# Performance work log

Measured on AMD Instinct MI355X. Metric: run time of the kernel, lower is better.

Reference implementation:

```python
import jax, jax.numpy as jnp
import numpy as np

B, C, H, W = 4, 64, 64, 64
INTER = max(1, C // 8)


def setup_inputs() -> dict:
    key = jax.random.key(0)
    ks = jax.random.split(key, 8)
    return {
        "x": jax.random.normal(ks[0], (B, C, H, W), dtype=jnp.float32),
        "Wq": jax.random.normal(ks[1], (INTER, C), dtype=jnp.float32) * 0.1,
        "bq": jax.random.normal(ks[2], (INTER,), dtype=jnp.float32) * 0.1,
        "Wk": jax.random.normal(ks[3], (INTER, C), dtype=jnp.float32) * 0.1,
        "bk": jax.random.normal(ks[4], (INTER,), dtype=jnp.float32) * 0.1,
        "Wv": jax.random.normal(ks[5], (C, C), dtype=jnp.float32) * 0.1,
        "bv": jax.random.normal(ks[6], (C,), dtype=jnp.float32) * 0.1,
        "gamma": jax.random.normal(ks[7], (1,), dtype=jnp.float32),
    }


def reference(x, Wq, bq, Wk, bk, Wv, bv, gamma):
    b, c, h, w = x.shape
    n = h * w
    xf = x.reshape(b, c, n)  # flatten spatial dims, [B, C, N]
    # 1x1 convs == per-pixel matmuls
    q = jnp.einsum('ic,bcn->bin', Wq, xf) + bq[None, :, None]  # [B, inter, N]
    k = jnp.einsum('ic,bcn->bin', Wk, xf) + bk[None, :, None]  # [B, inter, N]
    v = jnp.einsum('oc,bcn->bon', Wv, xf) + bv[None, :, None]  # [B, C, N]
    # energy[b,n,m] = sum_i q[b,i,n] * k[b,i,m]  (unscaled attention)
    energy = jnp.einsum('bin,bim->bnm', q, k)  # [B, N, N]
    attn = jax.nn.softmax(energy, axis=-1)
    # out[b,c,n] = sum_m v[b,c,m] * attn[b,n,m]
    out = jnp.einsum('bcm,bnm->bcn', v, attn).reshape(b, c, h, w)
    return gamma[0] * out + x
```

## Files before the change

kernel.cpp:

```cpp
#include <hip/hip_runtime.h>


#define NPIX 4096
typedef __attribute__((ext_vector_type(8))) short s8v;
typedef __attribute__((ext_vector_type(4))) float f4v;

static __device__ __forceinline__ unsigned short f2bf(float f) {
    union { float f; unsigned u; } v; v.f = f;
    unsigned r = v.u + 0x7FFFu + ((v.u >> 16) & 1u);
    return (unsigned short)(r >> 16);
}

extern "C" __global__ void __launch_bounds__(256, 4) qkv_kernel(
    const float* __restrict__ x,
    const float* __restrict__ Wq, const float* __restrict__ bq,
    const float* __restrict__ Wk, const float* __restrict__ bk,
    const float* __restrict__ Wv, const float* __restrict__ bv,
    unsigned short* __restrict__ qt, unsigned short* __restrict__ kt,
    unsigned short* __restrict__ vb)
{
    __shared__ float xs[64][17];
    __shared__ __align__(16) float wls[80][68];
    __shared__ float bls[80];
    const int t = threadIdx.x;
    const int b = blockIdx.x >> 8, n0 = (blockIdx.x & 255) << 4;

    for (int e = t; e < 1024; e += 256) {
        int c = e >> 4, j = e & 15;
        xs[c][j] = x[((b << 6) + c) * NPIX + n0 + j];
    }
    for (int e = t; e < 5120; e += 256) {
        int row = e >> 6, cc = e & 63;
        wls[row][cc] = (e < 512) ? Wq[e] : (e < 1024) ? Wk[e - 512] : Wv[e - 1024];
    }
    if (t < 80) bls[t] = (t < 8) ? bq[t] : (t < 16) ? bk[t - 8] : bv[t - 16];
    __syncthreads();

    const int j = t & 15, oh = t >> 4;
    float xr[64];
#pragma unroll
    for (int c = 0; c < 64; ++c) xr[c] = xs[c][j];

    const int n = n0 + j;
#pragma unroll
    for (int r = 0; r < 5; ++r) {
        const int row = oh * 5 + r;
        float acc = bls[row];
#pragma unroll
        for (int q = 0; q < 16; ++q) {
            float4 wv = *(const float4*)&wls[row][q * 4];
            acc += wv.x * xr[4*q] + wv.y * xr[4*q+1] + wv.z * xr[4*q+2] + wv.w * xr[4*q+3];
        }
        const unsigned short h = f2bf(acc);
        if (row < 8)       qt[(b * NPIX + n) * 8 + row] = h;
        else if (row < 16) kt[(b * NPIX + n) * 8 + row - 8] = h;
        else               vb[((b << 6) + (row - 16)) * NPIX + n] = h;
    }
}

extern "C" __global__ void __launch_bounds__(512, 4) attn_kernel(
    const unsigned short* __restrict__ qt, const unsigned short* __restrict__ kt,
    const unsigned short* __restrict__ vb,
    const float* __restrict__ x, const float* __restrict__ gamma_p,
    float* __restrict__ out)
{
    __shared__ __align__(16) unsigned short vls[4][64][64];
    __shared__ __align__(16) unsigned short pls[8][16][72];
    __shared__ float ored[2][128][17];
    __shared__ float Lred[4][2][16];

    const int t = threadIdx.x;
    const int w = t >> 6, lane = t & 63, g = lane >> 4, c16 = lane & 15;
    const int gg = w >> 1, wg = w & 1;
    const int bid = ((blockIdx.x & 7) << 6) + (blockIdx.x >> 3);
    const int b = bid >> 7, n0 = (bid & 127) << 5;

    const unsigned short* qtB = qt + b * NPIX * 8;
    const unsigned short* ktB = kt + b * NPIX * 8;
    const unsigned short* vbB = vb + (b << 6) * NPIX;

    s8v qfr = {0,0,0,0,0,0,0,0};
    if (g == 0) qfr = *(const s8v*)(qtB + (n0 + wg * 16 + c16) * 8);

    const int t2 = t & 127;
    const int vc = t2 >> 1, hh = t2 & 1;
    const int mbase = gg << 10;

    f4v accO[4];
#pragma unroll
    for (int cs = 0; cs < 4; ++cs) { accO[cs][0]=0.f; accO[cs][1]=0.f; accO[cs][2]=0.f; accO[cs][3]=0.f; }
    float lsum[4] = {0.f, 0.f, 0.f, 0.f};

    s8v vr[4], kf[4], kfn[4];
    {
        const unsigned short* vp = vbB + vc * NPIX + mbase + hh * 32;
        vr[0] = *(const s8v*)(vp);     vr[1] = *(const s8v*)(vp + 8);
        vr[2] = *(const s8v*)(vp + 16); vr[3] = *(const s8v*)(vp + 24);
#pragma unroll
        for (int ms = 0; ms < 4; ++ms) {
            s8v z = {0,0,0,0,0,0,0,0};
            kf[ms] = z;
            if (g == 0) kf[ms] = *(const s8v*)(ktB + (mbase + ms * 16 + c16) * 8);
        }
    }

    for (int ti = 0; ti < 16; ++ti) {
#pragma unroll
        for (int q = 0; q < 4; ++q) {
            const int pos = (hh * 4 + q) ^ (vc & 7);
            *(s8v*)&vls[gg][vc][pos * 8] = vr[q];
        }
        __syncthreads();

        if (ti < 15) {
            const int m1 = mbase + ((ti + 1) << 6);
            const unsigned short* vp = vbB + vc * NPIX + m1 + hh * 32;
            vr[0] = *(const s8v*)(vp);      vr[1] = *(const s8v*)(vp + 8);
            vr[2] = *(const s8v*)(vp + 16); vr[3] = *(const s8v*)(vp + 24);
#pragma unroll
            for (int ms = 0; ms < 4; ++ms) {
                s8v z = {0,0,0,0,0,0,0,0};
                kfn[ms] = z;
                if (g == 0) kfn[ms] = *(const s8v*)(ktB + (m1 + ms * 16 + c16) * 8);
            }
        }

        f4v sm[4];
#pragma unroll
        for (int ms = 0; ms < 4; ++ms) {
            f4v z; z[0]=0.f; z[1]=0.f; z[2]=0.f; z[3]=0.f;
            sm[ms] = __builtin_amdgcn_mfma_f32_16x16x32_bf16(qfr, kf[ms], z, 0, 0, 0);
        }

#pragma unroll
        for (int ms = 0; ms < 4; ++ms)
#pragma unroll
            for (int r = 0; r < 4; ++r) {
                float p = __expf(sm[ms][r]);
                lsum[r] += p;
                pls[w][g * 4 + r][ms * 16 + c16] = f2bf(p);
            }
        __builtin_amdgcn_wave_barrier();

        s8v pf0 = *(const s8v*)&pls[w][c16][g * 8];
        s8v pf1 = *(const s8v*)&pls[w][c16][32 + g * 8];

#pragma unroll
        for (int cs = 0; cs < 4; ++cs) {
            const int c = cs * 16 + c16;
            const int q0 = (g)     ^ (c16 & 7);
            const int q1 = (4 + g) ^ (c16 & 7);
            s8v vf0 = *(const s8v*)&vls[gg][c][q0 * 8];
            s8v vf1 = *(const s8v*)&vls[gg][c][q1 * 8];
            accO[cs] = __builtin_amdgcn_mfma_f32_16x16x32_bf16(vf0, pf0, accO[cs], 0, 0, 0);
            accO[cs] = __builtin_amdgcn_mfma_f32_16x16x32_bf16(vf1, pf1, accO[cs], 0, 0, 0);
        }
        __syncthreads();

#pragma unroll
        for (int ms = 0; ms < 4; ++ms) kf[ms] = kfn[ms];
    }

#pragma unroll
    for (int r = 0; r < 4; ++r) {
        float L = lsum[r];
        L += __shfl_xor(L, 1); L += __shfl_xor(L, 2);
        L += __shfl_xor(L, 4); L += __shfl_xor(L, 8);
        lsum[r] = L;
    }
    if (c16 == 0) {
#pragma unroll
        for (int r = 0; r < 4; ++r) Lred[gg][wg][g * 4 + r] = lsum[r];
    }

    const int s2 = t & 127;
    if (gg >= 2) {
#pragma unroll
        for (int cs = 0; cs < 4; ++cs)
#pragma unroll
            for (int r = 0; r < 4; ++r) ored[gg - 2][s2][cs * 4 + r] = accO[cs][r];
    }
    __syncthreads();
    if (gg < 2) {
#pragma unroll
        for (int cs = 0; cs < 4; ++cs)
#pragma unroll
            for (int r = 0; r < 4; ++r) accO[cs][r] += ored[gg][s2][cs * 4 + r];
    }
    __syncthreads();
    if (gg == 1) {
#pragma unroll
        for (int cs = 0; cs < 4; ++cs)
#pragma unroll
            for (int r = 0; r < 4; ++r) ored[0][s2][cs * 4 + r] = accO[cs][r];
    }
    __syncthreads();
    if (gg == 0) {
#pragma unroll
        for (int cs = 0; cs < 4; ++cs)
#pragma unroll
            for (int r = 0; r < 4; ++r) accO[cs][r] += ored[0][s2][cs * 4 + r];

        const float L = Lred[0][wg][c16] + Lred[1][wg][c16]
                      + Lred[2][wg][c16] + Lred[3][wg][c16];
        const float inv = 1.0f / L;
        const float gm = gamma_p[0];
        const int n = n0 + wg * 16 + c16;
#pragma unroll
        for (int cs = 0; cs < 4; ++cs)
#pragma unroll
            for (int r = 0; r < 4; ++r) {
                const int c = cs * 16 + g * 4 + r;
                const int gi = ((b << 6) + c) * NPIX + n;
                out[gi] = gm * (accO[cs][r] * inv) + x[gi];
            }
    }
}

extern "C" void kernel_launch(void* const* d_in, const int* in_sizes, int n_in,
                              void* d_out, int out_size, void* d_ws, size_t ws_size,
                              hipStream_t stream) {
    const float* x     = (const float*)d_in[0];
    const float* Wq    = (const float*)d_in[1];
    const float* bq    = (const float*)d_in[2];
    const float* Wk    = (const float*)d_in[3];
    const float* bk    = (const float*)d_in[4];
    const float* Wv    = (const float*)d_in[5];
    const float* bv    = (const float*)d_in[6];
    const float* gamma = (const float*)d_in[7];

    unsigned short* qt = (unsigned short*)d_ws;
    unsigned short* kt = qt + 4 * NPIX * 8;
    unsigned short* vb = kt + 4 * NPIX * 8;

    qkv_kernel<<<1024, 256, 0, stream>>>(x, Wq, bq, Wk, bk, Wv, bv, qt, kt, vb);
    attn_kernel<<<512, 512, 0, stream>>>(qt, kt, vb, x, gamma, (float*)d_out);
}
```

Baseline: 112.0 us.

## Restructure attention kernel: direct V fragment loads, 16-query tiles, exp2 softmax

Each attention block now handles 16 query pixels with 4 waves splitting the key range, up from 32 pixels with 8 waves. V fragments are loaded straight from global memory into registers and prefetched one tile ahead, which removes the LDS staging and both per-iteration __syncthreads. Q is pre-scaled by log2(e) in the projection kernel so the softmax can use a hardware exp2. The S MFMA operands are swapped so P can be written to LDS with packed bf16x2 stores, and the end-of-kernel reduction is a single LDS pass with vectorized float4 output. In exchange, V traffic from global/L2 is higher because there are twice as many blocks and no reuse of V through LDS.

```diff
diff --git a/kernel.cpp b/kernel.cpp
--- a/kernel.cpp
+++ b/kernel.cpp
@@ -1,7 +1,9 @@
 #include <hip/hip_runtime.h>
+#include <hip/hip_bf16.h>
 
 
 #define NPIX 4096
+#define LOG2E 1.44269504088896f
 typedef __attribute__((ext_vector_type(8))) short s8v;
 typedef __attribute__((ext_vector_type(4))) float f4v;
 
@@ -9,6 +11,17 @@
     union { float f; unsigned u; } v; v.f = f;
     unsigned r = v.u + 0x7FFFu + ((v.u >> 16) & 1u);
     return (unsigned short)(r >> 16);
+}
+static __device__ __forceinline__ unsigned pkbf2(float a, float b) {
+    __hip_bfloat162 h = __float22bfloat162_rn(make_float2(a, b));
+    return *reinterpret_cast<unsigned*>(&h);
+}
+static __device__ __forceinline__ float fexp2(float x) {
+#if __has_builtin(__builtin_amdgcn_exp2f)
+    return __builtin_amdgcn_exp2f(x);
+#else
+    return exp2f(x);
+#endif
 }
 
 extern "C" __global__ void __launch_bounds__(256, 4) qkv_kernel(
@@ -31,9 +44,10 @@
     }
     for (int e = t; e < 5120; e += 256) {
         int row = e >> 6, cc = e & 63;
-        wls[row][cc] = (e < 512) ? Wq[e] : (e < 1024) ? Wk[e - 512] : Wv[e - 1024];
-    }
-    if (t < 80) bls[t] = (t < 8) ? bq[t] : (t < 16) ? bk[t - 8] : bv[t - 16];
+        float wv = (e < 512) ? Wq[e] * LOG2E : (e < 1024) ? Wk[e - 512] : Wv[e - 1024];
+        wls[row][cc] = wv;
+    }
+    if (t < 80) bls[t] = (t < 8) ? bq[t] * LOG2E : (t < 16) ? bk[t - 8] : bv[t - 16];
     __syncthreads();
 
     const int j = t & 15, oh = t >> 4;
@@ -58,88 +72,76 @@
     }
 }
 
-extern "C" __global__ void __launch_bounds__(512, 4) attn_kernel(
+extern "C" __global__ void __launch_bounds__(256, 4) attn_kernel(
     const unsigned short* __restrict__ qt, const unsigned short* __restrict__ kt,
     const unsigned short* __restrict__ vb,
     const float* __restrict__ x, const float* __restrict__ gamma_p,
     float* __restrict__ out)
 {
-    __shared__ __align__(16) unsigned short vls[4][64][64];
-    __shared__ __align__(16) unsigned short pls[8][16][72];
-    __shared__ float ored[2][128][17];
-    __shared__ float Lred[4][2][16];
+    __shared__ __align__(16) unsigned short pls[4][16][72];
+    __shared__ __align__(16) float Ored[4][64][20];
+    __shared__ __align__(16) float Lr[4][16];
 
     const int t = threadIdx.x;
     const int w = t >> 6, lane = t & 63, g = lane >> 4, c16 = lane & 15;
-    const int gg = w >> 1, wg = w & 1;
-    const int bid = ((blockIdx.x & 7) << 6) + (blockIdx.x >> 3);
-    const int b = bid >> 7, n0 = (bid & 127) << 5;
+    const int raw = blockIdx.x;
+    const int sw = ((raw & 7) << 7) + (raw >> 3);
+    const int b = sw >> 8, n0 = (sw & 255) << 4;
 
     const unsigned short* qtB = qt + b * NPIX * 8;
     const unsigned short* ktB = kt + b * NPIX * 8;
     const unsigned short* vbB = vb + (b << 6) * NPIX;
 
     s8v qfr = {0,0,0,0,0,0,0,0};
-    if (g == 0) qfr = *(const s8v*)(qtB + (n0 + wg * 16 + c16) * 8);
-
-    const int t2 = t & 127;
-    const int vc = t2 >> 1, hh = t2 & 1;
-    const int mbase = gg << 10;
+    if (g == 0) qfr = *(const s8v*)(qtB + (n0 + c16) * 8);
+
+    const int mbase = w << 10;
+    const unsigned short* vrow = vbB + c16 * NPIX + g * 8;
 
     f4v accO[4];
 #pragma unroll
     for (int cs = 0; cs < 4; ++cs) { accO[cs][0]=0.f; accO[cs][1]=0.f; accO[cs][2]=0.f; accO[cs][3]=0.f; }
-    float lsum[4] = {0.f, 0.f, 0.f, 0.f};
-
-    s8v vr[4], kf[4], kfn[4];
-    {
-        const unsigned short* vp = vbB + vc * NPIX + mbase + hh * 32;
-        vr[0] = *(const s8v*)(vp);     vr[1] = *(const s8v*)(vp + 8);
-        vr[2] = *(const s8v*)(vp + 16); vr[3] = *(const s8v*)(vp + 24);
-#pragma unroll
-        for (int ms = 0; ms < 4; ++ms) {
-            s8v z = {0,0,0,0,0,0,0,0};
-            kf[ms] = z;
-            if (g == 0) kf[ms] = *(const s8v*)(ktB + (mbase + ms * 16 + c16) * 8);
-        }
+    float lsum = 0.f;
+
+    s8v kf[4], vf[8];
+#pragma unroll
+    for (int ms = 0; ms < 4; ++ms) {
+        s8v z = {0,0,0,0,0,0,0,0};
+        kf[ms] = z;
+        if (g == 0) kf[ms] = *(const s8v*)(ktB + (mbase + ms * 16 + c16) * 8);
+    }
+#pragma unroll
+    for (int cs = 0; cs < 4; ++cs) {
+        vf[cs*2+0] = *(const s8v*)(vrow + cs * 16 * NPIX + mbase);
+        vf[cs*2+1] = *(const s8v*)(vrow + cs * 16 * NPIX + mbase + 32);
     }
 
     for (int ti = 0; ti < 16; ++ti) {
-#pragma unroll
-        for (int q = 0; q < 4; ++q) {
-            const int pos = (hh * 4 + q) ^ (vc & 7);
-            *(s8v*)&vls[gg][vc][pos * 8] = vr[q];
-        }
-        __syncthreads();
-
-        if (ti < 15) {
-            const int m1 = mbase + ((ti + 1) << 6);
-            const unsigned short* vp = vbB + vc * NPIX + m1 + hh * 32;
-            vr[0] = *(const s8v*)(vp);      vr[1] = *(const s8v*)(vp + 8);
-            vr[2] = *(const s8v*)(vp + 16); vr[3] = *(const s8v*)(vp + 24);
-#pragma unroll
-            for (int ms = 0; ms < 4; ++ms) {
-                s8v z = {0,0,0,0,0,0,0,0};
-                kfn[ms] = z;
-                if (g == 0) kfn[ms] = *(const s8v*)(ktB + (m1 + ms * 16 + c16) * 8);
-            }
-        }
+        const int mg = mbase + (ti << 6);
 
         f4v sm[4];
 #pragma unroll
         for (int ms = 0; ms < 4; ++ms) {
             f4v z; z[0]=0.f; z[1]=0.f; z[2]=0.f; z[3]=0.f;
-            sm[ms] = __builtin_amdgcn_mfma_f32_16x16x32_bf16(qfr, kf[ms], z, 0, 0, 0);
-        }
-
-#pragma unroll
-        for (int ms = 0; ms < 4; ++ms)
-#pragma unroll
-            for (int r = 0; r < 4; ++r) {
-                float p = __expf(sm[ms][r]);
-                lsum[r] += p;
-                pls[w][g * 4 + r][ms * 16 + c16] = f2bf(p);
+            sm[ms] = __builtin_amdgcn_mfma_f32_16x16x32_bf16(kf[ms], qfr, z, 0, 0, 0);
+        }
+
+        if (ti < 15) {
+            const int m1 = mg + 64;
+#pragma unroll
+            for (int ms = 0; ms < 4; ++ms) {
+                if (g == 0) kf[ms] = *(const s8v*)(ktB + (m1 + ms * 16 + c16) * 8);
             }
+        }
+
+#pragma unroll
+        for (int ms = 0; ms < 4; ++ms) {
+            float p0 = fexp2(sm[ms][0]), p1 = fexp2(sm[ms][1]);
+            float p2 = fexp2(sm[ms][2]), p3 = fexp2(sm[ms][3]);
+            lsum += (p0 + p1) + (p2 + p3);
+            uint2 pk; pk.x = pkbf2(p0, p1); pk.y = pkbf2(p2, p3);
+            *(uint2*)&pls[w][c16][ms * 16 + g * 4] = pk;
+        }
         __builtin_amdgcn_wave_barrier();
 
         s8v pf0 = *(const s8v*)&pls[w][c16][g * 8];
@@ -147,73 +149,55 @@
 
 #pragma unroll
         for (int cs = 0; cs < 4; ++cs) {
-            const int c = cs * 16 + c16;
-            const int q0 = (g)     ^ (c16 & 7);
-            const int q1 = (4 + g) ^ (c16 & 7);
-            s8v vf0 = *(const s8v*)&vls[gg][c][q0 * 8];
-            s8v vf1 = *(const s8v*)&vls[gg][c][q1 * 8];
-            accO[cs] = __builtin_amdgcn_mfma_f32_16x16x32_bf16(vf0, pf0, accO[cs], 0, 0, 0);
-            accO[cs] = __builtin_amdgcn_mfma_f32_16x16x32_bf16(vf1, pf1, accO[cs], 0, 0, 0);
-        }
-        __syncthreads();
-
-#pragma unroll
-        for (int ms = 0; ms < 4; ++ms) kf[ms] = kfn[ms];
-    }
-
-#pragma unroll
-    for (int r = 0; r < 4; ++r) {
-        float L = lsum[r];
-        L += __shfl_xor(L, 1); L += __shfl_xor(L, 2);
-        L += __shfl_xor(L, 4); L += __shfl_xor(L, 8);
-        lsum[r] = L;
-    }
-    if (c16 == 0) {
-#pragma unroll
-        for (int r = 0; r < 4; ++r) Lred[gg][wg][g * 4 + r] = lsum[r];
-    }
-
-    const int s2 = t & 127;
-    if (gg >= 2) {
-#pragma unroll
-        for (int cs = 0; cs < 4; ++cs)
-#pragma unroll
-            for (int r = 0; r < 4; ++r) ored[gg - 2][s2][cs * 4 + r] = accO[cs][r];
-    }
+            accO[cs] = __builtin_amdgcn_mfma_f32_16x16x32_bf16(vf[cs*2+0], pf0, accO[cs], 0, 0, 0);
+            accO[cs] = __builtin_amdgcn_mfma_f32_16x16x32_bf16(vf[cs*2+1], pf1, accO[cs], 0, 0, 0);
+        }
+
+        if (ti < 15) {
+            const int m1 = mg + 64;
+#pragma unroll
+            for (int cs = 0; cs < 4; ++cs) {
+                vf[cs*2+0] = *(const s8v*)(vrow + cs * 16 * NPIX + m1);
+                vf[cs*2+1] = *(const s8v*)(vrow + cs * 16 * NPIX + m1 + 32);
+            }
+        }
+    }
+
+    lsum += __shfl_xor(lsum, 16);
+    lsum += __shfl_xor(lsum, 32);
+
+#pragma unroll
+    for (int cs = 0; cs < 4; ++cs)
+#pragma unroll
+        for (int r = 0; r < 4; ++r)
+            Ored[w][cs * 16 + g * 4 + r][c16] = accO[cs][r];
+    if (g == 0) Lr[w][c16] = lsum;
     __syncthreads();
-    if (gg < 2) {
-#pragma unroll
-        for (int cs = 0; cs < 4; ++cs)
-#pragma unroll
-            for (int r = 0; r < 4; ++r) accO[cs][r] += ored[gg][s2][cs * 4 + r];
-    }
-    __syncthreads();
-    if (gg == 1) {
-#pragma unroll
-        for (int cs = 0; cs < 4; ++cs)
-#pragma unroll
-            for (int r = 0; r < 4; ++r) ored[0][s2][cs * 4 + r] = accO[cs][r];
-    }
-    __syncthreads();
-    if (gg == 0) {
-#pragma unroll
-        for (int cs = 0; cs < 4; ++cs)
-#pragma unroll
-            for (int r = 0; r < 4; ++r) accO[cs][r] += ored[0][s2][cs * 4 + r];
-
-        const float L = Lred[0][wg][c16] + Lred[1][wg][c16]
-                      + Lred[2][wg][c16] + Lred[3][wg][c16];
-        const float inv = 1.0f / L;
+
+    {
+        const int c = t >> 2, nl = (t & 3) << 2;
+        float4 o = *(const float4*)&Ored[0][c][nl];
+        float4 o1 = *(const float4*)&Ored[1][c][nl];
+        float4 o2 = *(const float4*)&Ored[2][c][nl];
+        float4 o3 = *(const float4*)&Ored[3][c][nl];
+        o.x += o1.x + o2.x + o3.x;  o.y += o1.y + o2.y + o3.y;
+        o.z += o1.z + o2.z + o3.z;  o.w += o1.w + o2.w + o3.w;
+        float4 L0 = *(const float4*)&Lr[0][nl];
+        float4 L1 = *(const float4*)&Lr[1][nl];
+        float4 L2 = *(const float4*)&Lr[2][nl];
+        float4 L3 = *(const float4*)&Lr[3][nl];
+        float4 L;
+        L.x = L0.x + L1.x + L2.x + L3.x;  L.y = L0.y + L1.y + L2.y + L3.y;
+        L.z = L0.z + L1.z + L2.z + L3.z;  L.w = L0.w + L1.w + L2.w + L3.w;
         const float gm = gamma_p[0];
-        const int n = n0 + wg * 16 + c16;
-#pragma unroll
-        for (int cs = 0; cs < 4; ++cs)
-#pragma unroll
-            for (int r = 0; r < 4; ++r) {
-                const int c = cs * 16 + g * 4 + r;
-                const int gi = ((b << 6) + c) * NPIX + n;
-                out[gi] = gm * (accO[cs][r] * inv) + x[gi];
-            }
+        const int gi = ((b << 6) + c) * NPIX + n0 + nl;
+        float4 xv = *(const float4*)&x[gi];
+        float4 rs;
+        rs.x = gm * o.x / L.x + xv.x;
+        rs.y = gm * o.y / L.y + xv.y;
+        rs.z = gm * o.z / L.z + xv.z;
+        rs.w = gm * o.w / L.w + xv.w;
+        *(float4*)&out[gi] = rs;
     }
 }
 
@@ -234,5 +218,5 @@
     unsigned short* vb = kt + 4 * NPIX * 8;
 
     qkv_kernel<<<1024, 256, 0, stream>>>(x, Wq, bq, Wk, bk, Wv, bv, qt, kt, vb);
-    attn_kernel<<<512, 512, 0, stream>>>(qt, kt, vb, x, gamma, (float*)d_out);
-}
+    attn_kernel<<<1024, 256, 0, stream>>>(qt, kt, vb, x, gamma, (float*)d_out);
+}
```

Measured after the change: 146.9 us. +31.2%, slower.

## Fold log2e into Q weights, transpose score MFMA, pack bf16 P stores

Applied to the files above, without the earlier changes.

Scales Wq and bq by log2(e) in the projection kernel so the attention softmax can use the native exp2 instead of __expf. Swaps the operands of the QK MFMA so each lane holds four consecutive keys for one query. This lets P be packed into paired bf16 values and written as a single 8-byte store, and reduces the row-sum to a per-lane scalar combined with two shuffles. It also drops the kfn double buffer by reloading K right after its MFMAs, and aliases the output reduction scratch onto the V tile in shared memory to cut LDS usage.

```diff
diff --git a/kernel.cpp b/kernel.cpp
--- a/kernel.cpp
+++ b/kernel.cpp
@@ -1,7 +1,9 @@
 #include <hip/hip_runtime.h>
+#include <hip/hip_bf16.h>
 
 
 #define NPIX 4096
+#define LOG2E 1.44269504088896f
 typedef __attribute__((ext_vector_type(8))) short s8v;
 typedef __attribute__((ext_vector_type(4))) float f4v;
 
@@ -9,6 +11,17 @@
     union { float f; unsigned u; } v; v.f = f;
     unsigned r = v.u + 0x7FFFu + ((v.u >> 16) & 1u);
     return (unsigned short)(r >> 16);
+}
+static __device__ __forceinline__ unsigned pkbf2(float a, float b) {
+    __hip_bfloat162 h = __float22bfloat162_rn(make_float2(a, b));
+    return *reinterpret_cast<unsigned*>(&h);
+}
+static __device__ __forceinline__ float fexp2(float x) {
+#if __has_builtin(__builtin_amdgcn_exp2f)
+    return __builtin_amdgcn_exp2f(x);
+#else
+    return exp2f(x);
+#endif
 }
 
 extern "C" __global__ void __launch_bounds__(256, 4) qkv_kernel(
@@ -31,9 +44,10 @@
     }
     for (int e = t; e < 5120; e += 256) {
         int row = e >> 6, cc = e & 63;
-        wls[row][cc] = (e < 512) ? Wq[e] : (e < 1024) ? Wk[e - 512] : Wv[e - 1024];
-    }
-    if (t < 80) bls[t] = (t < 8) ? bq[t] : (t < 16) ? bk[t - 8] : bv[t - 16];
+        float wv = (e < 512) ? Wq[e] * LOG2E : (e < 1024) ? Wk[e - 512] : Wv[e - 1024];
+        wls[row][cc] = wv;
+    }
+    if (t < 80) bls[t] = (t < 8) ? bq[t] * LOG2E : (t < 16) ? bk[t - 8] : bv[t - 16];
     __syncthreads();
 
     const int j = t & 15, oh = t >> 4;
@@ -66,7 +80,6 @@
 {
     __shared__ __align__(16) unsigned short vls[4][64][64];
     __shared__ __align__(16) unsigned short pls[8][16][72];
-    __shared__ float ored[2][128][17];
     __shared__ float Lred[4][2][16];
 
     const int t = threadIdx.x;
@@ -89,12 +102,12 @@
     f4v accO[4];
 #pragma unroll
     for (int cs = 0; cs < 4; ++cs) { accO[cs][0]=0.f; accO[cs][1]=0.f; accO[cs][2]=0.f; accO[cs][3]=0.f; }
-    float lsum[4] = {0.f, 0.f, 0.f, 0.f};
-
-    s8v vr[4], kf[4], kfn[4];
+    float lsum = 0.f;
+
+    s8v vr[4], kf[4];
     {
         const unsigned short* vp = vbB + vc * NPIX + mbase + hh * 32;
-        vr[0] = *(const s8v*)(vp);     vr[1] = *(const s8v*)(vp + 8);
+        vr[0] = *(const s8v*)(vp);      vr[1] = *(const s8v*)(vp + 8);
         vr[2] = *(const s8v*)(vp + 16); vr[3] = *(const s8v*)(vp + 24);
 #pragma unroll
         for (int ms = 0; ms < 4; ++ms) {
@@ -112,34 +125,33 @@
         }
         __syncthreads();
 
+        const int m1 = mbase + ((ti + 1) << 6);
         if (ti < 15) {
-            const int m1 = mbase + ((ti + 1) << 6);
             const unsigned short* vp = vbB + vc * NPIX + m1 + hh * 32;
             vr[0] = *(const s8v*)(vp);      vr[1] = *(const s8v*)(vp + 8);
             vr[2] = *(const s8v*)(vp + 16); vr[3] = *(const s8v*)(vp + 24);
-#pragma unroll
-            for (int ms = 0; ms < 4; ++ms) {
-                s8v z = {0,0,0,0,0,0,0,0};
-                kfn[ms] = z;
-                if (g == 0) kfn[ms] = *(const s8v*)(ktB + (m1 + ms * 16 + c16) * 8);
-            }
         }
 
         f4v sm[4];
 #pragma unroll
         for (int ms = 0; ms < 4; ++ms) {
             f4v z; z[0]=0.f; z[1]=0.f; z[2]=0.f; z[3]=0.f;
-            sm[ms] = __builtin_amdgcn_mfma_f32_16x16x32_bf16(qfr, kf[ms], z, 0, 0, 0);
-        }
-
-#pragma unroll
-        for (int ms = 0; ms < 4; ++ms)
-#pragma unroll
-            for (int r = 0; r < 4; ++r) {
-                float p = __expf(sm[ms][r]);
-                lsum[r] += p;
-                pls[w][g * 4 + r][ms * 16 + c16] = f2bf(p);
-            }
+            sm[ms] = __builtin_amdgcn_mfma_f32_16x16x32_bf16(kf[ms], qfr, z, 0, 0, 0);
+        }
+        if (ti < 15) {
+#pragma unroll
+            for (int ms = 0; ms < 4; ++ms)
+                if (g == 0) kf[ms] = *(const s8v*)(ktB + (m1 + ms * 16 + c16) * 8);
+        }
+
+#pragma unroll
+        for (int ms = 0; ms < 4; ++ms) {
+            float p0 = fexp2(sm[ms][0]), p1 = fexp2(sm[ms][1]);
+            float p2 = fexp2(sm[ms][2]), p3 = fexp2(sm[ms][3]);
+            lsum += (p0 + p1) + (p2 + p3);
+            uint2 pk; pk.x = pkbf2(p0, p1); pk.y = pkbf2(p2, p3);
+            *(uint2*)&pls[w][c16][ms * 16 + g * 4] = pk;
+        }
         __builtin_amdgcn_wave_barrier();
 
         s8v pf0 = *(const s8v*)&pls[w][c16][g * 8];
@@ -156,23 +168,13 @@
             accO[cs] = __builtin_amdgcn_mfma_f32_16x16x32_bf16(vf1, pf1, accO[cs], 0, 0, 0);
         }
         __syncthreads();
-
-#pragma unroll
-        for (int ms = 0; ms < 4; ++ms) kf[ms] = kfn[ms];
-    }
-
-#pragma unroll
-    for (int r = 0; r < 4; ++r) {
-        float L = lsum[r];
-        L += __shfl_xor(L, 1); L += __shfl_xor(L, 2);
-        L += __shfl_xor(L, 4); L += __shfl_xor(L, 8);
-        lsum[r] = L;
-    }
-    if (c16 == 0) {
-#pragma unroll
-        for (int r = 0; r < 4; ++r) Lred[gg][wg][g * 4 + r] = lsum[r];
-    }
-
+    }
+
+    lsum += __shfl_xor(lsum, 16);
+    lsum += __shfl_xor(lsum, 32);
+    if (g == 0) Lred[gg][wg][c16] = lsum;
+
+    float (*ored)[128][17] = reinterpret_cast<float(*)[128][17]>(&vls[0][0][0]);
     const int s2 = t & 127;
     if (gg >= 2) {
 #pragma unroll
```

Measured after the change: 112.0 us. No clear change (+0.0%).
